# Kernel optimization log

Hardware: AMD Instinct MI355X
Metric: run time of the kernel (lower is better)

The kernel has to match this reference:

```python
import jax, jax.numpy as jnp
import numpy as np
from jax import lax

BLANK_ID = 0
NEG_INF = -1e10  # finite stand-in for log(0); module uses LOG_0 = -1e10

B, T, H, V, L = 32, 1000, 512, 2048, 100


def setup_inputs() -> dict:
    key = jax.random.key(0)
    k1, k2, k3, k4, k5, k6 = jax.random.split(key, 6)
    eouts = jax.random.normal(k1, (B, T, H), dtype=jnp.float32)
    W = jax.random.normal(k2, (V, H), dtype=jnp.float32) * (1.0 / np.sqrt(H))
    b = jax.random.normal(k3, (V,), dtype=jnp.float32) * 0.01
    ys = jax.random.randint(k4, (B, L), 1, V, dtype=jnp.int32)  # labels exclude blank=0
    ylens = jax.random.randint(k5, (B,), L // 2, L + 1, dtype=jnp.int32)
    # ensure T_b >= 2*L_b + 1 so every alignment is feasible
    elens = jnp.clip(jax.random.randint(k6, (B,), T // 2, T + 1, dtype=jnp.int32), 2 * L + 1, T)
    return {"eouts": eouts, "W": W, "b": b, "ys": ys, "elens": elens, "ylens": ylens}


def ctc_loss_sum(log_probs, ys, elens, ylens):
    """Batched CTC forward DP. log_probs: [B,T,V]; ys: [B,L]; returns sum loss."""
    Bb, Tt, Vv = log_probs.shape
    Ll = ys.shape[1]
    S = 2 * Ll + 1
    # extended label sequence: blank, y1, blank, y2, ..., blank
    ext = jnp.zeros((Bb, S), dtype=jnp.int32).at[:, 1::2].set(ys)
    # gather per-frame log-probs of extended labels: [B,T,S]
    lp_ext = jnp.take_along_axis(log_probs, jnp.broadcast_to(ext[:, None, :], (Bb, Tt, S)), axis=2)
    # s-2 skip allowed iff ext[s] != blank and ext[s] != ext[s-2]
    ext_m2 = jnp.pad(ext, ((0, 0), (2, 0)), constant_values=-1)[:, :S]
    skip_ok = (ext != BLANK_ID) & (ext != ext_m2)
    valid = jnp.arange(S)[None, :] < (2 * ylens[:, None] + 1)  # [B,S]

    a0 = jnp.full((Bb, S), NEG_INF, dtype=log_probs.dtype)
    a0 = a0.at[:, 0].set(lp_ext[:, 0, 0]).at[:, 1].set(lp_ext[:, 0, 1])
    a0 = jnp.where(valid, a0, NEG_INF)

    def step(a, lp_t):  # a: [B,S], lp_t: [B,S]
        a1 = a
        a2 = jnp.pad(a, ((0, 0), (1, 0)), constant_values=NEG_INF)[:, :S]
        a3 = jnp.where(skip_ok, jnp.pad(a, ((0, 0), (2, 0)), constant_values=NEG_INF)[:, :S], NEG_INF)
        new = jnp.logaddexp(jnp.logaddexp(a1, a2), a3) + lp_t
        new = jnp.where(valid, new, NEG_INF)
        return new, new

    _, alphas_rest = lax.scan(step, a0, jnp.swapaxes(lp_ext, 0, 1)[1:])  # [T-1,B,S]
    alphas = jnp.concatenate([a0[None], alphas_rest], axis=0)  # [T,B,S]

    a_final = alphas[elens - 1, jnp.arange(Bb)]  # [B,S]
    last = jnp.take_along_axis(a_final, (2 * ylens)[:, None], axis=1)[:, 0]
    prev = jnp.take_along_axis(a_final, (2 * ylens - 1)[:, None], axis=1)[:, 0]
    loss_b = -jnp.logaddexp(last, prev)
    # zero_infinity=True: replace non-finite (numerically huge) losses with 0
    loss_b = jnp.where(loss_b < -0.5 * NEG_INF, loss_b, 0.0)
    return jnp.sum(loss_b)


def reference(eouts, W, b, ys, elens, ylens):
    logits = jnp.einsum("bth,vh->btv", eouts, W) + b  # self.output(eouts)
    log_probs = jax.nn.log_softmax(logits, axis=-1)
    loss_ctc = ctc_loss_sum(log_probs, ys, elens, ylens) / eouts.shape[0]
    return loss_ctc
```

## Files before the change

kernel.cpp:

```cpp
#include <hip/hip_runtime.h>
#include <hip/hip_bf16.h>

#define B_ 32
#define T_ 1000
#define H_ 512
#define V_ 2048
#define L_ 100
#define M_ (B_*T_)
#define GSTRIDE 104
#define LOG2E 1.4426950408889634f
#define LSE_SHIFT 48.0f
#define BIAS60 1.152921504606847e18f

typedef __attribute__((ext_vector_type(8))) short bf16x8;
typedef __attribute__((ext_vector_type(4))) float f32x4;

#define AS_G(p)  ((const __attribute__((address_space(1))) unsigned int*)(p))
#define AS_L(p)  ((__attribute__((address_space(3))) unsigned int*)(p))

__device__ __forceinline__ unsigned short f2bf(float x) {
    unsigned int u; __builtin_memcpy(&u, &x, 4);
    unsigned int r = (u + 0x7fffu + ((u >> 16) & 1u)) >> 16;
    return (unsigned short)r;
}

__device__ __forceinline__ float dpp_shr1(float x) {
    int r = __builtin_amdgcn_update_dpp(0, __builtin_bit_cast(int, x), 0x138, 0xf, 0xf, false);
    return __builtin_bit_cast(float, r);
}
template<int CTRL>
__device__ __forceinline__ float fmax_dpp(float x) {
    int s = __builtin_amdgcn_update_dpp(0, __builtin_bit_cast(int, x), CTRL, 0xf, 0xf, false);
    return fmaxf(x, __builtin_bit_cast(float, s));
}
__device__ __forceinline__ float wave_max_nonneg(float x) {
    x = fmax_dpp<0x111>(x);
    x = fmax_dpp<0x112>(x);
    x = fmax_dpp<0x114>(x);
    x = fmax_dpp<0x118>(x);
    x = fmax_dpp<0x142>(x);
    x = fmax_dpp<0x143>(x);
    return __builtin_bit_cast(float, __builtin_amdgcn_readlane(__builtin_bit_cast(int, x), 63));
}

__global__ __launch_bounds__(256) void prep_kernel(
        const float* __restrict__ eouts, const float* __restrict__ W,
        unsigned short* __restrict__ eb, unsigned short* __restrict__ wb,
        float* __restrict__ Srow, float* __restrict__ out)
{
    const int E4 = M_*H_/4;
    const int W4 = V_*H_/4;
    const int S4 = M_/4;
    int idx = blockIdx.x*256 + threadIdx.x;
    if (idx == 0) out[0] = 0.f;
    if (idx < E4) {
        float4 v = ((const float4*)eouts)[idx];
        ushort4 o; o.x=f2bf(v.x); o.y=f2bf(v.y); o.z=f2bf(v.z); o.w=f2bf(v.w);
        ((ushort4*)eb)[idx] = o;
    } else if (idx < E4 + W4) {
        int j = idx - E4;
        float4 v = ((const float4*)W)[j];
        ushort4 o; o.x=f2bf(v.x); o.y=f2bf(v.y); o.z=f2bf(v.z); o.w=f2bf(v.w);
        ((ushort4*)wb)[j] = o;
    } else if (idx < E4 + W4 + S4) {
        int j = idx - E4 - W4;
        ((float4*)Srow)[j] = make_float4(0.f,0.f,0.f,0.f);
    }
}

__global__ __launch_bounds__(512, 1) void gemm_lse_kernel(
        const unsigned short* __restrict__ eb, const unsigned short* __restrict__ wb,
        const float* __restrict__ bias, float* __restrict__ Srow)
{
    __shared__ __align__(16) unsigned short Ab[2][256*64];
    __shared__ __align__(16) unsigned short Bb[2][256*64];
    __shared__ float rs[256];
    const int tid  = threadIdx.x;
    const int w    = tid >> 6;
    const int lane = tid & 63;
    const int m    = lane & 15;
    const int qh   = lane >> 4;
    const int wr   = w >> 2;
    const int wc   = w & 3;
    const int rl   = m & 7;
    const int lrow = lane >> 3;
    const int k8   = ((lane & 7) ^ lrow) * 8;
    const int nbase = blockIdx.x * 256;
    const int mbase = blockIdx.y * 256;

    if (tid < 256) rs[tid] = 0.f;

    f32x4 acc[8][4];
    #pragma unroll
    for (int i=0;i<8;i++)
        #pragma unroll
        for (int j=0;j<4;j++) acc[i][j] = (f32x4){0.f,0.f,0.f,0.f};
    bf16x8 af[2][2], bfr[4][2];

#define STAGE_A(sel, r, kt) do { \
        const unsigned short* _s = eb + (size_t)(mbase + (r)*64 + w*8 + lrow)*H_ + (kt)*64 + k8; \
        __builtin_amdgcn_global_load_lds(AS_G(_s), AS_L(&Ab[sel][((r)*64 + w*8)*64]), 16, 0, 0); \
    } while(0)
#define STAGE_B(sel, r, kt) do { \
        const unsigned short* _s = wb + (size_t)(nbase + (r)*64 + w*8 + lrow)*H_ + (kt)*64 + k8; \
        __builtin_amdgcn_global_load_lds(AS_G(_s), AS_L(&Bb[sel][((r)*64 + w*8)*64]), 16, 0, 0); \
    } while(0)

#define LOADB(sel) \
    _Pragma("unroll") \
    for (int ni=0; ni<4; ++ni) { \
        const int brow = wc*64 + ni*16 + m; \
        bfr[ni][0] = *(const bf16x8*)(&Bb[sel][brow*64 + ((qh ^ rl))*8]); \
        bfr[ni][1] = *(const bf16x8*)(&Bb[sel][brow*64 + (((4+qh) ^ rl))*8]); \
    }
#define LOADA(sel, qq) \
    _Pragma("unroll") \
    for (int mi2=0; mi2<2; ++mi2) { \
        const int arow = wr*128 + ((qq)*2+mi2)*16 + m; \
        af[mi2][0] = *(const bf16x8*)(&Ab[sel][arow*64 + ((qh ^ rl))*8]); \
        af[mi2][1] = *(const bf16x8*)(&Ab[sel][arow*64 + (((4+qh) ^ rl))*8]); \
    }
#define MFMA16(qq) \
    __builtin_amdgcn_s_setprio(1); \
    _Pragma("unroll") \
    for (int mi2=0; mi2<2; ++mi2) \
        _Pragma("unroll") \
        for (int ni=0; ni<4; ++ni) { \
            acc[(qq)*2+mi2][ni] = __builtin_amdgcn_mfma_f32_16x16x32_bf16(af[mi2][0], bfr[ni][0], acc[(qq)*2+mi2][ni], 0, 0, 0); \
            acc[(qq)*2+mi2][ni] = __builtin_amdgcn_mfma_f32_16x16x32_bf16(af[mi2][1], bfr[ni][1], acc[(qq)*2+mi2][ni], 0, 0, 0); \
        } \
    __builtin_amdgcn_s_setprio(0);
#define BARX() __builtin_amdgcn_s_barrier()
#define WAIT_LGKM() asm volatile("s_waitcnt lgkmcnt(0)" ::: "memory")

    STAGE_B(0,0,0); STAGE_B(0,1,0);
    STAGE_B(0,2,0); STAGE_B(0,3,0);
    STAGE_A(0,1,0); STAGE_A(0,3,0);
    STAGE_A(0,0,0); STAGE_A(0,2,0);
    STAGE_B(1,0,1); STAGE_B(1,1,1);
    STAGE_B(1,2,1); STAGE_B(1,3,1);
    STAGE_A(1,1,1); STAGE_A(1,3,1);
    asm volatile("s_waitcnt vmcnt(6)" ::: "memory");
    BARX();

    for (int it = 0; it < 4; ++it) {
        const int kt1 = 2*it + 1, kt2 = 2*it + 2, kt3 = 2*it + 3;
        const bool st = (it < 3);
        LOADB(0) LOADA(0,3)
        STAGE_A(1,0,kt1); STAGE_A(1,2,kt1);
        BARX(); WAIT_LGKM();
        MFMA16(3)
        BARX();
        LOADA(0,2)
        if (st) { STAGE_B(0,0,kt2); STAGE_B(0,1,kt2); }
        BARX(); WAIT_LGKM();
        MFMA16(2)
        BARX();
        LOADA(0,1)
        if (st) { STAGE_B(0,2,kt2); STAGE_B(0,3,kt2); }
        BARX(); WAIT_LGKM();
        MFMA16(1)
        BARX();
        LOADA(0,0)
        if (st) { STAGE_A(0,1,kt2); STAGE_A(0,3,kt2); }
        BARX(); WAIT_LGKM();
        MFMA16(0)
        if (st) { asm volatile("s_waitcnt vmcnt(6)" ::: "memory"); }
        else    { asm volatile("s_waitcnt vmcnt(0)" ::: "memory"); }
        BARX();
        LOADB(1) LOADA(1,3)
        if (st) { STAGE_A(0,0,kt2); STAGE_A(0,2,kt2); }
        BARX(); WAIT_LGKM();
        MFMA16(3)
        BARX();
        LOADA(1,2)
        if (st) { STAGE_B(1,0,kt3); STAGE_B(1,1,kt3); }
        BARX(); WAIT_LGKM();
        MFMA16(2)
        BARX();
        LOADA(1,1)
        if (st) { STAGE_B(1,2,kt3); STAGE_B(1,3,kt3); }
        BARX(); WAIT_LGKM();
        MFMA16(1)
        BARX();
        LOADA(1,0)
        if (st) { STAGE_A(1,1,kt3); STAGE_A(1,3,kt3); }
        BARX(); WAIT_LGKM();
        MFMA16(0)
        if (st) { asm volatile("s_waitcnt vmcnt(6)" ::: "memory"); }
        else    { asm volatile("s_waitcnt vmcnt(0)" ::: "memory"); }
        BARX();
    }

    float bv[4];
    #pragma unroll
    for (int ni=0;ni<4;ni++) bv[ni] = bias[nbase + wc*64 + ni*16 + m];
    #pragma unroll
    for (int mi=0;mi<8;mi++) {
        #pragma unroll
        for (int r=0;r<4;r++) {
            float s = 0.f;
            #pragma unroll
            for (int ni=0;ni<4;ni++)
                s += exp2f((acc[mi][ni][r] + bv[ni]) * LOG2E - LSE_SHIFT);
            s += __shfl_xor(s, 1);
            s += __shfl_xor(s, 2);
            s += __shfl_xor(s, 4);
            s += __shfl_xor(s, 8);
            if (m == 0) atomicAdd(&rs[wr*128 + mi*16 + qh*4 + r], s);
        }
    }
    __syncthreads();
    if (tid < 256) atomicAdd(&Srow[mbase + tid], rs[tid]);
#undef STAGE_A
#undef STAGE_B
#undef LOADB
#undef LOADA
#undef MFMA16
#undef BARX
#undef WAIT_LGKM
}

__global__ __launch_bounds__(256) void gather_mfma_kernel(
        const unsigned short* __restrict__ eb, const unsigned short* __restrict__ wb,
        const float* __restrict__ bias, const int* __restrict__ ys,
        const float* __restrict__ Srow, float* __restrict__ g)
{
    __shared__ __align__(16) unsigned short As[128*64];
    __shared__ __align__(16) unsigned short Bs[128*64];
    __shared__ float ls[128];
    const int tid  = threadIdx.x;
    const int w    = tid >> 6;
    const int lane = tid & 63;
    const int m    = lane & 15;
    const int q    = lane >> 4;
    const int wrow = w >> 1;
    const int wcol = w & 1;
    const int b    = blockIdx.y;
    const int tb   = blockIdx.x * 128;

    if (tid < 128) {
        int t = tb + tid;
        ls[tid] = (t < T_) ? (LSE_SHIFT + log2f(Srow[b*T_ + t])) : 0.f;
    }

    const int rbase = w*32 + (lane >> 3);
    const int k8    = (((lane & 7) ^ ((lane >> 3) & 7)) * 8);
    const int rl    = m & 7;

    int vrow[4];
    #pragma unroll
    for (int j=0;j<4;++j) {
        int labr = rbase + j*8;
        vrow[j] = (labr == 0 || labr > L_) ? 0 : ys[b*L_ + labr - 1];
    }
    int labc[4]; float bv[4];
    #pragma unroll
    for (int ni=0;ni<4;++ni) {
        int lab = wcol*64 + ni*16 + m;
        labc[ni] = lab;
        int v = (lab == 0 || lab > L_) ? 0 : ys[b*L_ + lab - 1];
        bv[ni] = bias[v];
    }

    f32x4 acc[4][4];
    #pragma unroll
    for (int i=0;i<4;i++)
        #pragma unroll
        for (int j=0;j<4;j++) acc[i][j] = (f32x4){0.f,0.f,0.f,0.f};

    for (int kc = 0; kc < 8; ++kc) {
        __syncthreads();
        #pragma unroll
        for (int j = 0; j < 4; ++j) {
            const unsigned short* ga = eb + (size_t)(b*T_ + tb + rbase + j*8)*H_ + kc*64 + k8;
            __builtin_amdgcn_global_load_lds(AS_G(ga), AS_L(As + (w*4+j)*512), 16, 0, 0);
            const unsigned short* gw = wb + (size_t)vrow[j]*H_ + kc*64 + k8;
            __builtin_amdgcn_global_load_lds(AS_G(gw), AS_L(Bs + (w*4+j)*512), 16, 0, 0);
        }
        __syncthreads();
        #pragma unroll
        for (int kk = 0; kk < 2; ++kk) {
            const int sw = ((kk*4 + q) ^ rl) * 8;
            bf16x8 af[4], bfr[4];
            #pragma unroll
            for (int mi=0;mi<4;mi++)
                af[mi] = *(const bf16x8*)(As + (wrow*8 + mi*2 + (m>>3))*512 + rl*64 + sw);
            #pragma unroll
            for (int ni=0;ni<4;ni++)
                bfr[ni] = *(const bf16x8*)(Bs + (wcol*8 + ni*2 + (m>>3))*512 + rl*64 + sw);
            #pragma unroll
            for (int mi=0;mi<4;mi++)
                #pragma unroll
                for (int ni=0;ni<4;ni++)
                    acc[mi][ni] = __builtin_amdgcn_mfma_f32_16x16x32_bf16(
                        af[mi], bfr[ni], acc[mi][ni], 0, 0, 0);
        }
    }

    #pragma unroll
    for (int mi=0;mi<4;mi++) {
        #pragma unroll
        for (int r=0;r<4;r++) {
            int trow = wrow*64 + mi*16 + q*4 + r;
            int t = tb + trow;
            float l2 = ls[trow];
            #pragma unroll
            for (int ni=0;ni<4;ni++) {
                if (t < T_ && labc[ni] <= L_) {
                    float p = exp2f((acc[mi][ni][r] + bv[ni]) * LOG2E - l2);
                    int off = (labc[ni] == 0) ? 0 : labc[ni] + 1;
                    g[(size_t)(b*T_ + t)*GSTRIDE + off] = p;
                }
            }
        }
    }
}

__global__ __launch_bounds__(128, 1) void ctc_dp_kernel(
        const float* __restrict__ g, const int* __restrict__ ys,
        const int* __restrict__ elens, const int* __restrict__ ylens,
        float* __restrict__ out)
{
    __shared__ __align__(16) float ring[2*2048];
    const int b    = blockIdx.x;
    const int tid  = threadIdx.x;
    const int wv   = tid >> 6;
    const int lane = tid & 63;
    const float* gb = g + (size_t)b * T_ * GSTRIDE;
    const int ylen = ylens[b];
    const int elen = elens[b];
    const int kmax = (elen - 1) >> 4;

    const int Sv   = 2*ylen + 1;
    const int s0   = 4*lane;
    const float msk0 = (s0   < Sv) ? 1.f : 0.f;
    const float msk1 = (s0+1 < Sv) ? 1.f : 0.f;
    const float msk2 = (s0+2 < Sv) ? 1.f : 0.f;
    const float msk3 = (s0+3 < Sv) ? 1.f : 0.f;
    const int l0 = 2*lane, l1 = 2*lane + 1;
    int i0 = min(max(l0,1), L_-1);
    int i1 = min(l1, L_-1);
    const float sk1 = (l0 >= 1 && l0 < L_ && ys[b*L_+i0] != ys[b*L_+i0-1]) ? 1.f : 0.f;
    const float sk3 = (l1 < L_        && ys[b*L_+i1] != ys[b*L_+i1-1]) ? 1.f : 0.f;

    float a0 = 0.f, a1 = 0.f, a2 = 0.f, a3 = 0.f, C2 = 0.f;
    if (wv == 0) {
        a0 = (lane == 0) ? gb[0] : 0.f;
        a1 = (lane == 0) ? gb[2] : 0.f;
    } else {
        #pragma unroll
        for (int s = 0; s < 8; ++s) {
            int srow = min(2*s, T_-2);
            __builtin_amdgcn_global_load_lds(AS_G(gb + (size_t)srow*GSTRIDE + 4*lane),
                                             AS_L(ring + s*256), 16, 0, 0);
        }
    }

    auto dpstep = [&](float p0, float p1, float p2, float p3) {
        float um1 = dpp_shr1(a3);
        float n0 = a0 + um1;
        float n1 = a1 + a0 + sk1*um1;
        float n2 = a2 + a1;
        float n3 = a3 + a2 + sk3*a1;
        a0 = n0*p0; a1 = n1*p1; a2 = n2*p2; a3 = n3*p3;
    };
    auto renorm = [&]() {
        float mm = wave_max_nonneg(fmaxf(fmaxf(a0,a1), fmaxf(a2,a3)));
        if (mm > 0.f) {
            float rr = fminf(__fdividef(BIAS60, mm), 3.0e38f);
            C2 -= __log2f(rr);
            a0 *= rr; a1 *= rr; a2 *= rr; a3 *= rr;
        }
    };

    __syncthreads();

    for (int k = 0; k <= kmax; ++k) {
        if (wv == 1) {
            if (k < kmax) {
                float* dset = ring + ((k+1) & 1)*2048;
                int pbase = 8*(k + 1);
                #pragma unroll
                for (int s = 0; s < 8; ++s) {
                    int srow = min(2*(pbase + s), T_-2);
                    __builtin_amdgcn_global_load_lds(AS_G(gb + (size_t)srow*GSTRIDE + 4*lane),
                                                     AS_L(dset + s*256), 16, 0, 0);
                }
            }
        } else {
            const float* sb = ring + (k & 1)*2048;
            float P0[16], P1[16], P2[16], P3[16];
            #pragma unroll
            for (int s = 0; s < 8; ++s) {
                const float* slot = sb + s*256;
                float pb0 = slot[0];
                float pb1 = slot[104];
                float2 lo = *(const float2*)(slot + 2  + 2*lane);
                float2 hi = *(const float2*)(slot + 106 + 2*lane);
                P0[2*s]   = pb0*msk0; P1[2*s]   = lo.x*msk1;
                P2[2*s]   = pb0*msk2; P3[2*s]   = lo.y*msk3;
                P0[2*s+1] = pb1*msk0; P1[2*s+1] = hi.x*msk1;
                P2[2*s+1] = pb1*msk2; P3[2*s+1] = hi.y*msk3;
            }
            const int t0 = 16*k;
            #pragma unroll
            for (int j = 0; j < 16; ++j) {
                int t = t0 + j;
                if (t > 0 && t < elen)
                    dpstep(P0[j], P1[j], P2[j], P3[j]);
                if ((j & 7) == 7) renorm();
            }
        }
        __syncthreads();
    }

    if (wv == 0) {
        int sA = 2*ylen, sB = sA - 1;
        float vA = __shfl((sA & 2) ? a2 : a0, sA >> 2);
        float vB = __shfl((sB & 2) ? a3 : a1, sB >> 2);
        if (lane == 0) {
            float sum = vA + vB;
            float loss = 0.f;
            if (sum > 0.f) {
                loss = -(log2f(sum) + C2) * 0.6931471805599453f;
                if (!(loss < 5e9f)) loss = 0.f;
            }
            atomicAdd(out, loss * (1.0f/B_));
        }
    }
}

extern "C" void kernel_launch(void* const* d_in, const int* in_sizes, int n_in,
                              void* d_out, int out_size, void* d_ws, size_t ws_size,
                              hipStream_t stream)
{
    const float* eouts = (const float*)d_in[0];
    const float* W     = (const float*)d_in[1];
    const float* bias  = (const float*)d_in[2];
    const int*   ys    = (const int*)d_in[3];
    const int*   elens = (const int*)d_in[4];
    const int*   ylens = (const int*)d_in[5];
    float* out = (float*)d_out;

    char* ws = (char*)d_ws;
    unsigned short* eb = (unsigned short*)ws;
    unsigned short* wb = (unsigned short*)(ws + 32768000);
    float* Srow        = (float*)(ws + 34865152);
    float* g           = (float*)(ws + 34993152);

    prep_kernel<<<17057, 256, 0, stream>>>(eouts, W, eb, wb, Srow, out);
    gemm_lse_kernel<<<dim3(8, 125), 512, 0, stream>>>(eb, wb, bias, Srow);
    gather_mfma_kernel<<<dim3(8, 32), 256, 0, stream>>>(eb, wb, bias, ys, Srow, g);
    ctc_dp_kernel<<<B_, 128, 0, stream>>>(g, ys, elens, ylens, out);
}
```

Before: 281.7 us.

## Make GEMM-LSE kernel persistent over M tiles with cross-tile prefetch

```diff
diff --git a/kernel.cpp b/kernel.cpp
--- a/kernel.cpp
+++ b/kernel.cpp
@@ -86,7 +86,9 @@
     const int lrow = lane >> 3;
     const int k8   = ((lane & 7) ^ lrow) * 8;
     const int nbase = blockIdx.x * 256;
-    const int mbase = blockIdx.y * 256;
+    const int ytile = blockIdx.y;
+    const int ntiles = (124 - ytile)/32 + 1;
+    int mb_cur = ytile * 256;
 
     if (tid < 256) rs[tid] = 0.f;
 
@@ -97,8 +99,8 @@
         for (int j=0;j<4;j++) acc[i][j] = (f32x4){0.f,0.f,0.f,0.f};
     bf16x8 af[2][2], bfr[4][2];
 
-#define STAGE_A(sel, r, kt) do { \
-        const unsigned short* _s = eb + (size_t)(mbase + (r)*64 + w*8 + lrow)*H_ + (kt)*64 + k8; \
+#define STAGE_A(sel, r, kt, mb) do { \
+        const unsigned short* _s = eb + (size_t)((mb) + (r)*64 + w*8 + lrow)*H_ + (kt)*64 + k8; \
         __builtin_amdgcn_global_load_lds(AS_G(_s), AS_L(&Ab[sel][((r)*64 + w*8)*64]), 16, 0, 0); \
     } while(0)
 #define STAGE_B(sel, r, kt) do { \
@@ -131,87 +133,107 @@
         } \
     __builtin_amdgcn_s_setprio(0);
 #define BARX() __builtin_amdgcn_s_barrier()
-#define WAIT_LGKM() asm volatile("s_waitcnt lgkmcnt(0)" ::: "memory")
+#define WAIT_LGKM() do { asm volatile("s_waitcnt lgkmcnt(0)" ::: "memory"); \
+                         __builtin_amdgcn_sched_barrier(0); } while(0)
 
     STAGE_B(0,0,0); STAGE_B(0,1,0);
     STAGE_B(0,2,0); STAGE_B(0,3,0);
-    STAGE_A(0,1,0); STAGE_A(0,3,0);
-    STAGE_A(0,0,0); STAGE_A(0,2,0);
+    STAGE_A(0,1,0,mb_cur); STAGE_A(0,3,0,mb_cur);
+    STAGE_A(0,0,0,mb_cur); STAGE_A(0,2,0,mb_cur);
     STAGE_B(1,0,1); STAGE_B(1,1,1);
     STAGE_B(1,2,1); STAGE_B(1,3,1);
-    STAGE_A(1,1,1); STAGE_A(1,3,1);
+    STAGE_A(1,1,1,mb_cur); STAGE_A(1,3,1,mb_cur);
     asm volatile("s_waitcnt vmcnt(6)" ::: "memory");
     BARX();
 
-    for (int it = 0; it < 4; ++it) {
-        const int kt1 = 2*it + 1, kt2 = 2*it + 2, kt3 = 2*it + 3;
-        const bool st = (it < 3);
-        LOADB(0) LOADA(0,3)
-        STAGE_A(1,0,kt1); STAGE_A(1,2,kt1);
-        BARX(); WAIT_LGKM();
-        MFMA16(3)
-        BARX();
-        LOADA(0,2)
-        if (st) { STAGE_B(0,0,kt2); STAGE_B(0,1,kt2); }
-        BARX(); WAIT_LGKM();
-        MFMA16(2)
-        BARX();
-        LOADA(0,1)
-        if (st) { STAGE_B(0,2,kt2); STAGE_B(0,3,kt2); }
-        BARX(); WAIT_LGKM();
-        MFMA16(1)
-        BARX();
-        LOADA(0,0)
-        if (st) { STAGE_A(0,1,kt2); STAGE_A(0,3,kt2); }
-        BARX(); WAIT_LGKM();
-        MFMA16(0)
-        if (st) { asm volatile("s_waitcnt vmcnt(6)" ::: "memory"); }
-        else    { asm volatile("s_waitcnt vmcnt(0)" ::: "memory"); }
-        BARX();
-        LOADB(1) LOADA(1,3)
-        if (st) { STAGE_A(0,0,kt2); STAGE_A(0,2,kt2); }
-        BARX(); WAIT_LGKM();
-        MFMA16(3)
-        BARX();
-        LOADA(1,2)
-        if (st) { STAGE_B(1,0,kt3); STAGE_B(1,1,kt3); }
-        BARX(); WAIT_LGKM();
-        MFMA16(2)
-        BARX();
-        LOADA(1,1)
-        if (st) { STAGE_B(1,2,kt3); STAGE_B(1,3,kt3); }
-        BARX(); WAIT_LGKM();
-        MFMA16(1)
-        BARX();
-        LOADA(1,0)
-        if (st) { STAGE_A(1,1,kt3); STAGE_A(1,3,kt3); }
-        BARX(); WAIT_LGKM();
-        MFMA16(0)
-        if (st) { asm volatile("s_waitcnt vmcnt(6)" ::: "memory"); }
-        else    { asm volatile("s_waitcnt vmcnt(0)" ::: "memory"); }
-        BARX();
-    }
-
-    float bv[4];
-    #pragma unroll
-    for (int ni=0;ni<4;ni++) bv[ni] = bias[nbase + wc*64 + ni*16 + m];
-    #pragma unroll
-    for (int mi=0;mi<8;mi++) {
-        #pragma unroll
-        for (int r=0;r<4;r++) {
-            float s = 0.f;
-            #pragma unroll
-            for (int ni=0;ni<4;ni++)
-                s += exp2f((acc[mi][ni][r] + bv[ni]) * LOG2E - LSE_SHIFT);
-            s += __shfl_xor(s, 1);
-            s += __shfl_xor(s, 2);
-            s += __shfl_xor(s, 4);
-            s += __shfl_xor(s, 8);
-            if (m == 0) atomicAdd(&rs[wr*128 + mi*16 + qh*4 + r], s);
-        }
-    }
-    __syncthreads();
-    if (tid < 256) atomicAdd(&Srow[mbase + tid], rs[tid]);
+    #pragma unroll 1
+    for (int mt = 0; mt < ntiles; ++mt) {
+        const int mb_nxt = (ytile + 32*(mt+1)) * 256;
+        #pragma unroll 1
+        for (int it = 0; it < 4; ++it) {
+            const bool last = (mt == ntiles-1) && (it == 3);
+            const int k1 = 2*it + 1;
+            const int k2 = (2*it + 2) & 7;
+            const int k3 = (2*it + 3) & 7;
+            const int mbs = (it < 3) ? mb_cur : mb_nxt;
+            LOADB(0) LOADA(0,3)
+            STAGE_A(1,0,k1,mb_cur); STAGE_A(1,2,k1,mb_cur);
+            BARX(); WAIT_LGKM();
+            MFMA16(3)
+            BARX();
+            LOADA(0,2)
+            if (!last) { STAGE_B(0,0,k2); STAGE_B(0,1,k2); }
+            BARX(); WAIT_LGKM();
+            MFMA16(2)
+            BARX();
+            LOADA(0,1)
+            if (!last) { STAGE_B(0,2,k2); STAGE_B(0,3,k2); }
+            BARX(); WAIT_LGKM();
+            MFMA16(1)
+            BARX();
+            LOADA(0,0)
+            if (!last) { STAGE_A(0,1,k2,mbs); STAGE_A(0,3,k2,mbs); }
+            BARX(); WAIT_LGKM();
+            MFMA16(0)
+            if (!last) { asm volatile("s_waitcnt vmcnt(6)" ::: "memory"); }
+            else       { asm volatile("s_waitcnt vmcnt(0)" ::: "memory"); }
+            BARX();
+            LOADB(1) LOADA(1,3)
+            if (!last) { STAGE_A(0,0,k2,mbs); STAGE_A(0,2,k2,mbs); }
+            BARX(); WAIT_LGKM();
+            MFMA16(3)
+            BARX();
+            LOADA(1,2)
+            if (!last) { STAGE_B(1,0,k3); STAGE_B(1,1,k3); }
+            BARX(); WAIT_LGKM();
+            MFMA16(2)
+            BARX();
+            LOADA(1,1)
+            if (!last) { STAGE_B(1,2,k3); STAGE_B(1,3,k3); }
+            BARX(); WAIT_LGKM();
+            MFMA16(1)
+            BARX();
+            LOADA(1,0)
+            if (!last) { STAGE_A(1,1,k3,mbs); STAGE_A(1,3,k3,mbs); }
+            BARX(); WAIT_LGKM();
+            MFMA16(0)
+            if (!last) { asm volatile("s_waitcnt vmcnt(6)" ::: "memory"); }
+            else       { asm volatile("s_waitcnt vmcnt(0)" ::: "memory"); }
+            BARX();
+        }
+
+        {
+            float bv[4];
+            #pragma unroll
+            for (int ni=0;ni<4;ni++) bv[ni] = bias[nbase + wc*64 + ni*16 + m];
+            #pragma unroll
+            for (int mi=0;mi<8;mi++) {
+                #pragma unroll
+                for (int r=0;r<4;r++) {
+                    float s = 0.f;
+                    #pragma unroll
+                    for (int ni=0;ni<4;ni++)
+                        s += exp2f((acc[mi][ni][r] + bv[ni]) * LOG2E - LSE_SHIFT);
+                    s += __shfl_xor(s, 1);
+                    s += __shfl_xor(s, 2);
+                    s += __shfl_xor(s, 4);
+                    s += __shfl_xor(s, 8);
+                    if (m == 0) atomicAdd(&rs[wr*128 + mi*16 + qh*4 + r], s);
+                }
+            }
+            WAIT_LGKM();
+            BARX();
+            if (tid < 256) {
+                atomicAdd(&Srow[mb_cur + tid], rs[tid]);
+                rs[tid] = 0.f;
+            }
+            #pragma unroll
+            for (int i=0;i<8;i++)
+                #pragma unroll
+                for (int j=0;j<4;j++) acc[i][j] = (f32x4){0.f,0.f,0.f,0.f};
+        }
+        mb_cur = mb_nxt;
+    }
 #undef STAGE_A
 #undef STAGE_B
 #undef LOADB
@@ -450,7 +472,7 @@
     float* g           = (float*)(ws + 34993152);
 
     prep_kernel<<<17057, 256, 0, stream>>>(eouts, W, eb, wb, Srow, out);
-    gemm_lse_kernel<<<dim3(8, 125), 512, 0, stream>>>(eb, wb, bias, Srow);
+    gemm_lse_kernel<<<dim3(8, 32), 512, 0, stream>>>(eb, wb, bias, Srow);
     gather_mfma_kernel<<<dim3(8, 32), 256, 0, stream>>>(eb, wb, bias, ys, Srow, g);
     ctc_dp_kernel<<<B_, 128, 0, stream>>>(g, ys, elens, ylens, out);
 }
```

Result: no change. 276.8 us (-1.8%).
